# Kernel tuning notes

Hardware: AMD Instinct MI355X
Metric: run time of the kernel (lower is better)

The kernel has to match this reference:

```python
import jax, jax.numpy as jnp
import numpy as np
import math

NEG_INF = -1e30  # stand-in for float('-inf'); softmax/logsumexp treat it identically


def _fnoise(x):
    # factorized NoisyNet transform f(x) = sign(x) * sqrt(|x|)
    return jnp.sign(x) * jnp.sqrt(jnp.abs(x))


def setup_inputs() -> dict:
    B, T, D, E = 4, 4096, 2048, 16
    key = jax.random.key(0)
    ks = jax.random.split(key, 6)
    sigma_init = 0.4 / math.sqrt(D)  # sigma_zero / sqrt(in_features)
    return {
        "mh_output": jax.random.normal(ks[0], (B, T, D), dtype=jnp.float32),
        "weight": jax.random.normal(ks[1], (E, D), dtype=jnp.float32) * 0.02,
        "sigma_weight": jnp.full((E, D), sigma_init, dtype=jnp.float32),
        "bias": jax.random.normal(ks[2], (E,), dtype=jnp.float32) * 0.02,
        "sigma_bias": jnp.full((E,), sigma_init, dtype=jnp.float32),
        "eps_in": jax.random.normal(ks[3], (D,), dtype=jnp.float32),
        "eps_out": jax.random.normal(ks[4], (E,), dtype=jnp.float32),
    }


def reference(mh_output, weight, sigma_weight, bias, sigma_bias, eps_in, eps_out):
    top_k = 2
    E = weight.shape[0]

    # NoisyFactorizedLinear: W' = W + sigma_W * (f(eps_out) f(eps_in)^T)
    f_in = _fnoise(eps_in)            # [D]
    f_out = _fnoise(eps_out)          # [E]
    w_noisy = weight + sigma_weight * (f_out[:, None] * f_in[None, :])  # [E, D]
    b_noisy = bias + sigma_bias * f_out                                 # [E]
    logits = jnp.einsum("btd,ed->bte", mh_output, w_noisy) + b_noisy    # [B,T,E]
    # dropout(p=0.125) is identity in eval mode

    top_vals, indices = jax.lax.top_k(logits, top_k)                    # [B,T,k]
    # scatter top-k back into a -inf-filled tensor == mask of selected experts
    keep = jnp.sum(jax.nn.one_hot(indices, E, dtype=jnp.bool_), axis=-2)  # [B,T,E]
    sparse_logits = jnp.where(keep, logits, NEG_INF)

    router_output = jax.nn.softmax(sparse_logits, axis=-1)

    # z-loss: mean(logsumexp(sparse_logits, -1)^2); only top-k entries survive
    lse = jax.scipy.special.logsumexp(top_vals, axis=-1)                # [B,T]
    z_loss = jnp.mean(lse ** 2)

    return router_output, indices, z_loss
```

## Files before the change

kernel.cpp:

```cpp
#include <hip/hip_runtime.h>
#include <math.h>

#define NROWS 16384
#define DDIM  2048
#define NEXP  16
#define RBLOCKS 1024
#define WPB 4
#define ZN (RBLOCKS * WPB)

__device__ __forceinline__ float fnoise(float x) {
    return copysignf(sqrtf(fabsf(x)), x);
}

__device__ __forceinline__ void async_copy16(const float4* g, float4* l) {
    __builtin_amdgcn_global_load_lds(
        (const __attribute__((address_space(1))) void*)g,
        (__attribute__((address_space(3))) void*)l, 16, 0, 0);
}


__global__ void prep_kernel(const float* __restrict__ weight,
                            const float* __restrict__ sigma_weight,
                            const float* __restrict__ bias,
                            const float* __restrict__ sigma_bias,
                            const float* __restrict__ eps_in,
                            const float* __restrict__ eps_out,
                            float* __restrict__ w_noisy,
                            float* __restrict__ b_noisy) {
    int idx = blockIdx.x * blockDim.x + threadIdx.x;
    int e = idx >> 11;
    int d = idx & (DDIM - 1);
    float fi = fnoise(eps_in[d]);
    float fo = fnoise(eps_out[e]);
    w_noisy[idx] = weight[idx] + sigma_weight[idx] * fo * fi;
    if (idx < NEXP) {
        b_noisy[idx] = bias[idx] + sigma_bias[idx] * fnoise(eps_out[idx]);
    }
}

__global__ __launch_bounds__(256, 4) void router_kernel(
        const float* __restrict__ x,
        const float* __restrict__ w_noisy,
        const float* __restrict__ b_noisy,
        float* __restrict__ out_router,
        float* __restrict__ out_idx,
        float* __restrict__ zpart) {
    __shared__ float4 wlds[2][NEXP * 64];

    const int tid  = threadIdx.x;
    const int wv   = tid >> 6;
    const int lane = tid & 63;

    const int rowBase = blockIdx.x * 16 + wv * 4;
    const float4* xr0 = (const float4*)(x + (size_t)(rowBase + 0) * DDIM);
    const float4* xr1 = (const float4*)(x + (size_t)(rowBase + 1) * DDIM);
    const float4* xr2 = (const float4*)(x + (size_t)(rowBase + 2) * DDIM);
    const float4* xr3 = (const float4*)(x + (size_t)(rowBase + 3) * DDIM);
    const float4* wsrc = (const float4*)w_noisy;

    float acc[64];
    #pragma unroll
    for (int i = 0; i < 64; ++i) acc[i] = 0.0f;

    float4 xbuf[2][4];

    #pragma unroll
    for (int j = 0; j < 4; ++j) {
        int e = j * 4 + wv;
        async_copy16(wsrc + (size_t)e * 512 + lane,
                     &wlds[0][j * 256 + wv * 64]);
    }
    xbuf[0][0] = xr0[lane];
    xbuf[0][1] = xr1[lane];
    xbuf[0][2] = xr2[lane];
    xbuf[0][3] = xr3[lane];
    __syncthreads();

    #pragma unroll
    for (int c = 0; c < 8; ++c) {
        const int cur = c & 1;
        const int nxt = cur ^ 1;
        if (c < 7) {
            int p = (c + 1) * 64 + lane;
            xbuf[nxt][0] = xr0[p];
            xbuf[nxt][1] = xr1[p];
            xbuf[nxt][2] = xr2[p];
            xbuf[nxt][3] = xr3[p];
            #pragma unroll
            for (int j = 0; j < 4; ++j) {
                int e = j * 4 + wv;
                async_copy16(wsrc + (size_t)e * 512 + (c + 1) * 64 + lane,
                             &wlds[nxt][j * 256 + wv * 64]);
            }
        }
        #pragma unroll
        for (int e = 0; e < 16; ++e) {
            float4 w = wlds[cur][e * 64 + lane];
            float s0 = acc[0 * 16 + e];
            float s1 = acc[1 * 16 + e];
            float s2 = acc[2 * 16 + e];
            float s3 = acc[3 * 16 + e];
            s0 = fmaf(xbuf[cur][0].x, w.x, s0); s0 = fmaf(xbuf[cur][0].y, w.y, s0);
            s0 = fmaf(xbuf[cur][0].z, w.z, s0); s0 = fmaf(xbuf[cur][0].w, w.w, s0);
            s1 = fmaf(xbuf[cur][1].x, w.x, s1); s1 = fmaf(xbuf[cur][1].y, w.y, s1);
            s1 = fmaf(xbuf[cur][1].z, w.z, s1); s1 = fmaf(xbuf[cur][1].w, w.w, s1);
            s2 = fmaf(xbuf[cur][2].x, w.x, s2); s2 = fmaf(xbuf[cur][2].y, w.y, s2);
            s2 = fmaf(xbuf[cur][2].z, w.z, s2); s2 = fmaf(xbuf[cur][2].w, w.w, s2);
            s3 = fmaf(xbuf[cur][3].x, w.x, s3); s3 = fmaf(xbuf[cur][3].y, w.y, s3);
            s3 = fmaf(xbuf[cur][3].z, w.z, s3); s3 = fmaf(xbuf[cur][3].w, w.w, s3);
            acc[0 * 16 + e] = s0;
            acc[1 * 16 + e] = s1;
            acc[2 * 16 + e] = s2;
            acc[3 * 16 + e] = s3;
        }
        if (c < 7) __syncthreads();
    }

    #pragma unroll
    for (int half = 32; half >= 1; half >>= 1) {
        #pragma unroll
        for (int i = 0; i < half; ++i) {
            bool hi = (lane & half) != 0;
            float keep = hi ? acc[i + half] : acc[i];
            float send = hi ? acc[i] : acc[i + half];
            float recv = __shfl_xor(send, half, 64);
            acc[i] = keep + recv;
        }
    }

    const int e = lane & 15;
    const int r = lane >> 4;
    const int row = rowBase + r;
    float logit = acc[0] + b_noisy[e];

    float m1 = logit; int i1 = e;
    #pragma unroll
    for (int off = 8; off >= 1; off >>= 1) {
        float om = __shfl_xor(m1, off, 64);
        int   oi = __shfl_xor(i1, off, 64);
        if (om > m1 || (om == m1 && oi < i1)) { m1 = om; i1 = oi; }
    }
    float v2 = (e == i1) ? -3.4e38f : logit;
    float m2 = v2; int i2 = e;
    #pragma unroll
    for (int off = 8; off >= 1; off >>= 1) {
        float om = __shfl_xor(m2, off, 64);
        int   oi = __shfl_xor(i2, off, 64);
        if (om > m2 || (om == m2 && oi < i2)) { m2 = om; i2 = oi; }
    }

    float t = expf(m2 - m1);
    float p1 = 1.0f / (1.0f + t);
    float val = (e == i1) ? p1 : ((e == i2) ? t * p1 : 0.0f);
    out_router[(size_t)rowBase * NEXP + lane] = val;

    if (e < 2) {
        out_idx[(size_t)row * 2 + e] = (float)((e == 0) ? i1 : i2);
    }

    float zv = 0.0f;
    if (e == 0) {
        float lse = m1 + log1pf(t);
        zv = lse * lse;
    }
    zv += __shfl_xor(zv, 16, 64);
    zv += __shfl_xor(zv, 32, 64);
    if (lane == 0) {
        zpart[blockIdx.x * WPB + wv] = zv;
    }
}

__global__ void finalize_kernel(const float* __restrict__ zpart,
                                float* __restrict__ out) {
    __shared__ float ws4[4];
    int tid = threadIdx.x;
    float s = 0.0f;
    for (int i = tid; i < ZN; i += 256) s += zpart[i];
    #pragma unroll
    for (int off = 32; off >= 1; off >>= 1) s += __shfl_xor(s, off, 64);
    if ((tid & 63) == 0) ws4[tid >> 6] = s;
    __syncthreads();
    if (tid == 0) {
        float total = ws4[0] + ws4[1] + ws4[2] + ws4[3];
        out[NROWS * NEXP + NROWS * 2] = total * (1.0f / (float)NROWS);
    }
}

extern "C" void kernel_launch(void* const* d_in, const int* in_sizes, int n_in,
                              void* d_out, int out_size, void* d_ws, size_t ws_size,
                              hipStream_t stream) {
    const float* mh      = (const float*)d_in[0];
    const float* weight  = (const float*)d_in[1];
    const float* sigw    = (const float*)d_in[2];
    const float* bias    = (const float*)d_in[3];
    const float* sigb    = (const float*)d_in[4];
    const float* eps_in  = (const float*)d_in[5];
    const float* eps_out = (const float*)d_in[6];

    float* out      = (float*)d_out;
    float* w_noisy  = (float*)d_ws;
    float* b_noisy  = w_noisy + NEXP * DDIM;
    float* zpart    = w_noisy + 32800;

    prep_kernel<<<(NEXP * DDIM) / 256, 256, 0, stream>>>(
        weight, sigw, bias, sigb, eps_in, eps_out, w_noisy, b_noisy);

    router_kernel<<<RBLOCKS, 256, 0, stream>>>(
        mh, w_noisy, b_noisy, out, out + NROWS * NEXP, zpart);

    finalize_kernel<<<1, 256, 0, stream>>>(zpart, out);
}
```

Before: 212.3 us.

## Double block size to 8 waves and stage 128-column weight chunks per barrier

The router kernel now runs 512 threads per block, each block covering 32 rows, so every weight tile staged in LDS is reused by twice as many waves. Each LDS stage now holds 128 float4 columns per expert and feeds two x sub-chunks, which halves the number of __syncthreads barriers. The cost is double the LDS per block (64 KB total across both buffers), which may cap occupancy. Larger blocks also leave fewer blocks to balance across the CUs.

```diff
diff --git a/kernel.cpp b/kernel.cpp
--- a/kernel.cpp
+++ b/kernel.cpp
@@ -4,8 +4,8 @@
 #define NROWS 16384
 #define DDIM  2048
 #define NEXP  16
-#define RBLOCKS 1024
-#define WPB 4
+#define RBLOCKS 512
+#define WPB 8
 #define ZN (RBLOCKS * WPB)
 
 __device__ __forceinline__ float fnoise(float x) {
@@ -38,20 +38,20 @@
     }
 }
 
-__global__ __launch_bounds__(256, 4) void router_kernel(
+__global__ __launch_bounds__(512, 4) void router_kernel(
         const float* __restrict__ x,
         const float* __restrict__ w_noisy,
         const float* __restrict__ b_noisy,
         float* __restrict__ out_router,
         float* __restrict__ out_idx,
         float* __restrict__ zpart) {
-    __shared__ float4 wlds[2][NEXP * 64];
+    __shared__ float4 wlds[2][NEXP * 128];
 
     const int tid  = threadIdx.x;
     const int wv   = tid >> 6;
     const int lane = tid & 63;
 
-    const int rowBase = blockIdx.x * 16 + wv * 4;
+    const int rowBase = blockIdx.x * 32 + wv * 4;
     const float4* xr0 = (const float4*)(x + (size_t)(rowBase + 0) * DDIM);
     const float4* xr1 = (const float4*)(x + (size_t)(rowBase + 1) * DDIM);
     const float4* xr2 = (const float4*)(x + (size_t)(rowBase + 2) * DDIM);
@@ -66,9 +66,9 @@
 
     #pragma unroll
     for (int j = 0; j < 4; ++j) {
-        int e = j * 4 + wv;
-        async_copy16(wsrc + (size_t)e * 512 + lane,
-                     &wlds[0][j * 256 + wv * 64]);
+        int fb = j * 512 + wv * 64;
+        async_copy16(wsrc + (size_t)(fb >> 7) * 512 + (fb & 127) + lane,
+                     &wlds[0][fb]);
     }
     xbuf[0][0] = xr0[lane];
     xbuf[0][1] = xr1[lane];
@@ -77,43 +77,52 @@
     __syncthreads();
 
     #pragma unroll
-    for (int c = 0; c < 8; ++c) {
-        const int cur = c & 1;
-        const int nxt = cur ^ 1;
-        if (c < 7) {
-            int p = (c + 1) * 64 + lane;
-            xbuf[nxt][0] = xr0[p];
-            xbuf[nxt][1] = xr1[p];
-            xbuf[nxt][2] = xr2[p];
-            xbuf[nxt][3] = xr3[p];
+    for (int q = 0; q < 4; ++q) {
+        const int cb = q & 1;
+        const int nb = cb ^ 1;
+        if (q < 3) {
             #pragma unroll
             for (int j = 0; j < 4; ++j) {
-                int e = j * 4 + wv;
-                async_copy16(wsrc + (size_t)e * 512 + (c + 1) * 64 + lane,
-                             &wlds[nxt][j * 256 + wv * 64]);
+                int fb = j * 512 + wv * 64;
+                async_copy16(wsrc + (size_t)(fb >> 7) * 512 + (q + 1) * 128
+                                 + (fb & 127) + lane,
+                             &wlds[nb][fb]);
             }
         }
         #pragma unroll
-        for (int e = 0; e < 16; ++e) {
-            float4 w = wlds[cur][e * 64 + lane];
-            float s0 = acc[0 * 16 + e];
-            float s1 = acc[1 * 16 + e];
-            float s2 = acc[2 * 16 + e];
-            float s3 = acc[3 * 16 + e];
-            s0 = fmaf(xbuf[cur][0].x, w.x, s0); s0 = fmaf(xbuf[cur][0].y, w.y, s0);
-            s0 = fmaf(xbuf[cur][0].z, w.z, s0); s0 = fmaf(xbuf[cur][0].w, w.w, s0);
-            s1 = fmaf(xbuf[cur][1].x, w.x, s1); s1 = fmaf(xbuf[cur][1].y, w.y, s1);
-            s1 = fmaf(xbuf[cur][1].z, w.z, s1); s1 = fmaf(xbuf[cur][1].w, w.w, s1);
-            s2 = fmaf(xbuf[cur][2].x, w.x, s2); s2 = fmaf(xbuf[cur][2].y, w.y, s2);
-            s2 = fmaf(xbuf[cur][2].z, w.z, s2); s2 = fmaf(xbuf[cur][2].w, w.w, s2);
-            s3 = fmaf(xbuf[cur][3].x, w.x, s3); s3 = fmaf(xbuf[cur][3].y, w.y, s3);
-            s3 = fmaf(xbuf[cur][3].z, w.z, s3); s3 = fmaf(xbuf[cur][3].w, w.w, s3);
-            acc[0 * 16 + e] = s0;
-            acc[1 * 16 + e] = s1;
-            acc[2 * 16 + e] = s2;
-            acc[3 * 16 + e] = s3;
+        for (int h = 0; h < 2; ++h) {
+            const int c = 2 * q + h;
+            const int xc = c & 1;
+            const int xn = xc ^ 1;
+            if (c < 7) {
+                int p = (c + 1) * 64 + lane;
+                xbuf[xn][0] = xr0[p];
+                xbuf[xn][1] = xr1[p];
+                xbuf[xn][2] = xr2[p];
+                xbuf[xn][3] = xr3[p];
+            }
+            #pragma unroll
+            for (int e = 0; e < 16; ++e) {
+                float4 w = wlds[cb][e * 128 + h * 64 + lane];
+                float s0 = acc[0 * 16 + e];
+                float s1 = acc[1 * 16 + e];
+                float s2 = acc[2 * 16 + e];
+                float s3 = acc[3 * 16 + e];
+                s0 = fmaf(xbuf[xc][0].x, w.x, s0); s0 = fmaf(xbuf[xc][0].y, w.y, s0);
+                s0 = fmaf(xbuf[xc][0].z, w.z, s0); s0 = fmaf(xbuf[xc][0].w, w.w, s0);
+                s1 = fmaf(xbuf[xc][1].x, w.x, s1); s1 = fmaf(xbuf[xc][1].y, w.y, s1);
+                s1 = fmaf(xbuf[xc][1].z, w.z, s1); s1 = fmaf(xbuf[xc][1].w, w.w, s1);
+                s2 = fmaf(xbuf[xc][2].x, w.x, s2); s2 = fmaf(xbuf[xc][2].y, w.y, s2);
+                s2 = fmaf(xbuf[xc][2].z, w.z, s2); s2 = fmaf(xbuf[xc][2].w, w.w, s2);
+                s3 = fmaf(xbuf[xc][3].x, w.x, s3); s3 = fmaf(xbuf[xc][3].y, w.y, s3);
+                s3 = fmaf(xbuf[xc][3].z, w.z, s3); s3 = fmaf(xbuf[xc][3].w, w.w, s3);
+                acc[0 * 16 + e] = s0;
+                acc[1 * 16 + e] = s1;
+                acc[2 * 16 + e] = s2;
+                acc[3 * 16 + e] = s3;
+            }
         }
-        if (c < 7) __syncthreads();
+        if (q < 3) __syncthreads();
     }
 
     #pragma unroll
@@ -205,7 +214,7 @@
     prep_kernel<<<(NEXP * DDIM) / 256, 256, 0, stream>>>(
         weight, sigw, bias, sigb, eps_in, eps_out, w_noisy, b_noisy);
 
-    router_kernel<<<RBLOCKS, 256, 0, stream>>>(
+    router_kernel<<<RBLOCKS, 512, 0, stream>>>(
         mh, w_noisy, b_noisy, out, out + NROWS * NEXP, zpart);
 
     finalize_kernel<<<1, 256, 0, stream>>>(zpart, out);
```

Measured after the change: 209.6 us. No clear change (-1.3%).

## Stage full noisy weight in LDS once per larger block and drop per-chunk syncs

Applied to the files above, without the earlier changes.

The router kernel now uses 512-thread blocks covering 32 rows each. The whole 16x2048 noisy weight matrix goes into LDS in one upfront async load, replacing the double-buffered per-chunk weight copies and their per-chunk barriers. Activation loads move to a 3-deep register prefetch. This halves the total L2-to-LDS weight traffic and removes seven block barriers. In exchange, the 128KB LDS footprint likely allows only one block per CU, which lowers occupancy, and the whole weight load must finish before any compute starts.

```diff
diff --git a/kernel.cpp b/kernel.cpp
--- a/kernel.cpp
+++ b/kernel.cpp
@@ -4,8 +4,8 @@
 #define NROWS 16384
 #define DDIM  2048
 #define NEXP  16
-#define RBLOCKS 1024
-#define WPB 4
+#define RBLOCKS 512
+#define WPB 8
 #define ZN (RBLOCKS * WPB)
 
 __device__ __forceinline__ float fnoise(float x) {
@@ -38,20 +38,20 @@
     }
 }
 
-__global__ __launch_bounds__(256, 4) void router_kernel(
+__global__ __launch_bounds__(512, 2) void router_kernel(
         const float* __restrict__ x,
         const float* __restrict__ w_noisy,
         const float* __restrict__ b_noisy,
         float* __restrict__ out_router,
         float* __restrict__ out_idx,
         float* __restrict__ zpart) {
-    __shared__ float4 wlds[2][NEXP * 64];
+    __shared__ float4 wlds[NEXP * 512];
 
     const int tid  = threadIdx.x;
     const int wv   = tid >> 6;
     const int lane = tid & 63;
 
-    const int rowBase = blockIdx.x * 16 + wv * 4;
+    const int rowBase = blockIdx.x * 32 + wv * 4;
     const float4* xr0 = (const float4*)(x + (size_t)(rowBase + 0) * DDIM);
     const float4* xr1 = (const float4*)(x + (size_t)(rowBase + 1) * DDIM);
     const float4* xr2 = (const float4*)(x + (size_t)(rowBase + 2) * DDIM);
@@ -62,40 +62,33 @@
     #pragma unroll
     for (int i = 0; i < 64; ++i) acc[i] = 0.0f;
 
-    float4 xbuf[2][4];
-
-    #pragma unroll
-    for (int j = 0; j < 4; ++j) {
-        int e = j * 4 + wv;
-        async_copy16(wsrc + (size_t)e * 512 + lane,
-                     &wlds[0][j * 256 + wv * 64]);
-    }
-    xbuf[0][0] = xr0[lane];
-    xbuf[0][1] = xr1[lane];
-    xbuf[0][2] = xr2[lane];
-    xbuf[0][3] = xr3[lane];
+    float4 xbuf[3][4];
+
+    #pragma unroll
+    for (int j = 0; j < 16; ++j) {
+        int fb = j * 512 + wv * 64;
+        async_copy16(wsrc + fb + lane, &wlds[fb]);
+    }
+    xbuf[0][0] = xr0[lane];       xbuf[0][1] = xr1[lane];
+    xbuf[0][2] = xr2[lane];       xbuf[0][3] = xr3[lane];
+    xbuf[1][0] = xr0[64 + lane];  xbuf[1][1] = xr1[64 + lane];
+    xbuf[1][2] = xr2[64 + lane];  xbuf[1][3] = xr3[64 + lane];
     __syncthreads();
 
     #pragma unroll
     for (int c = 0; c < 8; ++c) {
-        const int cur = c & 1;
-        const int nxt = cur ^ 1;
-        if (c < 7) {
-            int p = (c + 1) * 64 + lane;
-            xbuf[nxt][0] = xr0[p];
-            xbuf[nxt][1] = xr1[p];
-            xbuf[nxt][2] = xr2[p];
-            xbuf[nxt][3] = xr3[p];
-            #pragma unroll
-            for (int j = 0; j < 4; ++j) {
-                int e = j * 4 + wv;
-                async_copy16(wsrc + (size_t)e * 512 + (c + 1) * 64 + lane,
-                             &wlds[nxt][j * 256 + wv * 64]);
-            }
+        const int cur = c % 3;
+        const int pre = (c + 2) % 3;
+        if (c < 6) {
+            int p = (c + 2) * 64 + lane;
+            xbuf[pre][0] = xr0[p];
+            xbuf[pre][1] = xr1[p];
+            xbuf[pre][2] = xr2[p];
+            xbuf[pre][3] = xr3[p];
         }
         #pragma unroll
         for (int e = 0; e < 16; ++e) {
-            float4 w = wlds[cur][e * 64 + lane];
+            float4 w = wlds[e * 512 + c * 64 + lane];
             float s0 = acc[0 * 16 + e];
             float s1 = acc[1 * 16 + e];
             float s2 = acc[2 * 16 + e];
@@ -113,7 +106,6 @@
             acc[2 * 16 + e] = s2;
             acc[3 * 16 + e] = s3;
         }
-        if (c < 7) __syncthreads();
     }
 
     #pragma unroll
@@ -205,7 +197,7 @@
     prep_kernel<<<(NEXP * DDIM) / 256, 256, 0, stream>>>(
         weight, sigw, bias, sigb, eps_in, eps_out, w_noisy, b_noisy);
 
-    router_kernel<<<RBLOCKS, 256, 0, stream>>>(
+    router_kernel<<<RBLOCKS, 512, 0, stream>>>(
         mh, w_noisy, b_noisy, out, out + NROWS * NEXP, zpart);
 
     finalize_kernel<<<1, 256, 0, stream>>>(zpart, out);
```

Measured after the change: 212.5 us. Within noise of the previous version (+0.1%).
